# Kernel tuning notes

Hardware: AMD Instinct MI355X
Metric: run time of the kernel (lower is better)

## Reference

```python
import jax, jax.numpy as jnp
import numpy as np

D = 512
B = 8
S1 = 2048
S2 = 2048


def _rope_cos_sin(seq_len, dim, dtype=jnp.float32):
    half = dim // 2
    inv_freq = 1.0 / (10000.0 ** (jnp.arange(half, dtype=jnp.float32) / half))
    t = jnp.arange(seq_len, dtype=jnp.float32)
    freqs = jnp.outer(t, inv_freq)                      # [S, D/2]
    emb = jnp.concatenate([freqs, freqs], axis=-1)      # [S, D]
    return jnp.cos(emb).astype(dtype), jnp.sin(emb).astype(dtype)


def _rotate_half(x):
    half = x.shape[-1] // 2
    return jnp.concatenate([-x[..., half:], x[..., :half]], axis=-1)


def _apply_rope(x, cos, sin):
    # x: [B, S, D]; cos/sin: [S, D]
    return x * cos[None, :, :] + _rotate_half(x) * sin[None, :, :]


def setup_inputs() -> dict:
    key = jax.random.key(0)
    ks = jax.random.split(key, 12)
    s = 1.0 / np.sqrt(D)
    return {
        "h1": jax.random.normal(ks[0], (B, S1, D), dtype=jnp.float32),
        "h2": jax.random.normal(ks[1], (B, S2, D), dtype=jnp.float32),
        "Wq": jax.random.normal(ks[2], (D, D), dtype=jnp.float32) * s,
        "bq": jnp.zeros((D,), dtype=jnp.float32),
        "Wk": jax.random.normal(ks[3], (D, D), dtype=jnp.float32) * s,
        "bk": jnp.zeros((D,), dtype=jnp.float32),
        "Wv": jax.random.normal(ks[4], (D, D), dtype=jnp.float32) * s,
        "bv": jnp.zeros((D,), dtype=jnp.float32),
        "Wo": jax.random.normal(ks[5], (D, D), dtype=jnp.float32) * s,
        "bo": jnp.zeros((D,), dtype=jnp.float32),
    }


def reference(h1, h2, Wq, bq, Wk, bk, Wv, bv, Wo, bo):
    d = h1.shape[-1]
    # Linear projections (torch Linear: x @ W.T + b)
    q = jnp.einsum("bsd,ed->bse", h1, Wq) + bq
    k = jnp.einsum("bsd,ed->bse", h2, Wk) + bk
    v = jnp.einsum("bsd,ed->bse", h2, Wv) + bv
    # RoPE on full hidden dim (single head)
    cos_q, sin_q = _rope_cos_sin(q.shape[1], d)
    cos_k, sin_k = _rope_cos_sin(k.shape[1], d)
    q = _apply_rope(q, cos_q, sin_q)
    k = _apply_rope(k, cos_k, sin_k)
    # scaled dot-product attention with full score matrix (faithful to source)
    energy = jnp.einsum("bqd,bkd->bqk", q, k) / jnp.sqrt(jnp.float32(d))
    attn = jax.nn.softmax(energy, axis=-1)
    out = jnp.einsum("bqk,bkd->bqd", attn, v)
    return jnp.einsum("bsd,ed->bse", out, Wo) + bo
```

## Files before the change

kernel.cpp:

```cpp
#include <hip/hip_runtime.h>
#include <stdint.h>

#define SCALE_E 0.044194173824159216f
#define LOG2_10000 13.287712379549449f
#define MCONST 8.0f

typedef __bf16 bf16x8 __attribute__((ext_vector_type(8)));
typedef float  f32x4  __attribute__((ext_vector_type(4)));

#define MFMA16(a, b, c) __builtin_amdgcn_mfma_f32_16x16x32_bf16((a), (b), (c), 0, 0, 0)

__device__ __forceinline__ void gload_lds16(const void* gp, void* lp) {
  __builtin_amdgcn_global_load_lds(
      reinterpret_cast<const uint32_t __attribute__((address_space(1)))*>(
          reinterpret_cast<uintptr_t>(gp)),
      reinterpret_cast<uint32_t __attribute__((address_space(3)))*>(
          reinterpret_cast<uintptr_t>(lp)),
      16, 0, 0);
}

__global__ __launch_bounds__(256) void gemm_split(
    const float* __restrict__ A, const float* __restrict__ W,
    const float* __restrict__ bias, float* __restrict__ C, int M)
{
  __shared__ __align__(16) __bf16 Als[2 * 512 * 8];
  __shared__ __align__(16) __bf16 Wls[2 * 512 * 8];

  const int t    = threadIdx.x;
  const int lane = t & 63;
  const int w    = t >> 6;
  const int m    = lane & 15;
  const int quad = lane >> 4;
  const int mw   = w & 1;
  const int nw   = w >> 1;
  const int m0   = blockIdx.y * 128;
  const int n0   = blockIdx.x * 128;

  const float* Ap0 = A + (size_t)(m0 + w * 16 + m) * 512 + quad * 8;
  const float* Ap1 = A + (size_t)(m0 + (w + 4) * 16 + m) * 512 + quad * 8;
  const float* Wp0 = W + (size_t)(n0 + w * 16 + m) * 512 + quad * 8;
  const float* Wp1 = W + (size_t)(n0 + (w + 4) * 16 + m) * 512 + quad * 8;

  f32x4 acc[4][4] = {};

  float4 ra[4], rw_[4];
  ra[0] = *(const float4*)(Ap0);     ra[1] = *(const float4*)(Ap0 + 4);
  ra[2] = *(const float4*)(Ap1);     ra[3] = *(const float4*)(Ap1 + 4);
  rw_[0] = *(const float4*)(Wp0);    rw_[1] = *(const float4*)(Wp0 + 4);
  rw_[2] = *(const float4*)(Wp1);    rw_[3] = *(const float4*)(Wp1 + 4);

  for (int kt = 0; kt < 512; kt += 32) {
    __syncthreads();
    #pragma unroll
    for (int h = 0; h < 2; ++h) {
      int slot = t + 256 * h;
      float v[8] = {ra[2*h].x, ra[2*h].y, ra[2*h].z, ra[2*h].w,
                    ra[2*h+1].x, ra[2*h+1].y, ra[2*h+1].z, ra[2*h+1].w};
      float u[8] = {rw_[2*h].x, rw_[2*h].y, rw_[2*h].z, rw_[2*h].w,
                    rw_[2*h+1].x, rw_[2*h+1].y, rw_[2*h+1].z, rw_[2*h+1].w};
      bf16x8 ah, al, bh, bl;
      #pragma unroll
      for (int j = 0; j < 8; ++j) {
        __bf16 hv = (__bf16)v[j];
        ah[j] = hv; al[j] = (__bf16)(v[j] - (float)hv);
        __bf16 hu = (__bf16)u[j];
        bh[j] = hu; bl[j] = (__bf16)(u[j] - (float)hu);
      }
      *(bf16x8*)&Als[(size_t)slot * 8]         = ah;
      *(bf16x8*)&Als[(size_t)(512 + slot) * 8] = al;
      *(bf16x8*)&Wls[(size_t)slot * 8]         = bh;
      *(bf16x8*)&Wls[(size_t)(512 + slot) * 8] = bl;
    }
    __syncthreads();

    if (kt + 32 < 512) {
      ra[0] = *(const float4*)(Ap0 + kt + 32);  ra[1] = *(const float4*)(Ap0 + kt + 36);
      ra[2] = *(const float4*)(Ap1 + kt + 32);  ra[3] = *(const float4*)(Ap1 + kt + 36);
      rw_[0] = *(const float4*)(Wp0 + kt + 32); rw_[1] = *(const float4*)(Wp0 + kt + 36);
      rw_[2] = *(const float4*)(Wp1 + kt + 32); rw_[3] = *(const float4*)(Wp1 + kt + 36);
    }

    bf16x8 ah[4], al[4], bh[4], bl[4];
    #pragma unroll
    for (int mt = 0; mt < 4; ++mt) {
      ah[mt] = *(const bf16x8*)&Als[(size_t)((mw * 4 + mt) * 64 + lane) * 8];
      al[mt] = *(const bf16x8*)&Als[(size_t)(512 + (mw * 4 + mt) * 64 + lane) * 8];
    }
    #pragma unroll
    for (int nt = 0; nt < 4; ++nt) {
      bh[nt] = *(const bf16x8*)&Wls[(size_t)((nw * 4 + nt) * 64 + lane) * 8];
      bl[nt] = *(const bf16x8*)&Wls[(size_t)(512 + (nw * 4 + nt) * 64 + lane) * 8];
    }
    #pragma unroll
    for (int mt = 0; mt < 4; ++mt)
      #pragma unroll
      for (int nt = 0; nt < 4; ++nt) {
        acc[mt][nt] = MFMA16(al[mt], bh[nt], acc[mt][nt]);
        acc[mt][nt] = MFMA16(ah[mt], bl[nt], acc[mt][nt]);
        acc[mt][nt] = MFMA16(ah[mt], bh[nt], acc[mt][nt]);
      }
  }

  float bv[4];
  #pragma unroll
  for (int nt = 0; nt < 4; ++nt) bv[nt] = bias[n0 + (nw * 4 + nt) * 16 + m];

  #pragma unroll
  for (int mt = 0; mt < 4; ++mt)
    #pragma unroll
    for (int r = 0; r < 4; ++r) {
      size_t row = m0 + (mw * 4 + mt) * 16 + quad * 4 + r;
      float* cp = C + row * 512 + n0;
      #pragma unroll
      for (int nt = 0; nt < 4; ++nt)
        cp[(nw * 4 + nt) * 16 + m] = acc[mt][nt][r] + bv[nt];
    }
}

__global__ __launch_bounds__(256) void rope_cast(
    const float* __restrict__ X, __bf16* __restrict__ Y, float scale)
{
  const int row = blockIdx.x;
  const int s = row & 2047;
  const int j = threadIdx.x;
  const float* p = X + (size_t)row * 512;
  __bf16* q = Y + (size_t)row * 512;
  float invf = exp2f((float)j * (-LOG2_10000 / 256.0f));
  float ang = (float)s * invf;
  float c = cosf(ang), sn = sinf(ang);
  float x1 = p[j], x2 = p[j + 256];
  q[j]       = (__bf16)((x1 * c - x2 * sn) * scale);
  q[j + 256] = (__bf16)((x2 * c + x1 * sn) * scale);
}

__global__ __launch_bounds__(256) void cast_transpose_v(
    const float* __restrict__ V, __bf16* __restrict__ Vt)
{
  __shared__ float tile[32][33];
  const int b  = blockIdx.z;
  const int s0 = blockIdx.x * 32;
  const int d0 = blockIdx.y * 32;
  const float* Vb = V + (size_t)b * 2048 * 512;
  __bf16* Vtb = Vt + (size_t)b * 512 * 2048;

  #pragma unroll
  for (int r = 0; r < 4; ++r) {
    int s = s0 + threadIdx.y + 8 * r;
    tile[threadIdx.y + 8 * r][threadIdx.x] = Vb[(size_t)s * 512 + d0 + threadIdx.x];
  }
  __syncthreads();
  #pragma unroll
  for (int r = 0; r < 4; ++r) {
    int d = d0 + threadIdx.y + 8 * r;
    Vtb[(size_t)d * 2048 + s0 + threadIdx.x] = (__bf16)tile[threadIdx.x][threadIdx.y + 8 * r];
  }
}

__global__ __launch_bounds__(512, 2) void attn_mfma(
    const __bf16* __restrict__ Qb, const __bf16* __restrict__ Kb,
    const __bf16* __restrict__ Vt, float* __restrict__ O)
{
  __shared__ __align__(16) __bf16 Kbuf[2][2048 * 8];
  __shared__ __align__(16) __bf16 Vbuf[2048 * 8];
  __shared__ __align__(16) __bf16 Ps[2048];
  __shared__ float l_sh[128];

  const int t    = threadIdx.x;
  const int b    = blockIdx.x >> 5;
  const int q0   = (blockIdx.x & 31) * 64;
  const int w    = t >> 6;
  const int lane = t & 63;
  const int m    = lane & 15;
  const int quad = lane >> 4;
  const int rw   = w >> 1;
  const int kw   = w & 1;

  const __bf16* Kbase = Kb + (size_t)b * 2048 * 512;
  const __bf16* Vbase = Vt + (size_t)b * 512 * 2048;

  const __bf16* qrow = Qb + ((size_t)b * 2048 + q0 + rw * 16 + m) * 512 + quad * 8;
  bf16x8 qf[16];
  #pragma unroll
  for (int kb = 0; kb < 16; ++kb) qf[kb] = *(const bf16x8*)(qrow + kb * 32);

  f32x4 o_acc[4][4] = {};
  float l_acc[4] = {};

  #pragma unroll
  for (int i = 0; i < 4; ++i) {
    const int j = w * 4 + i;
    gload_lds16(Kbase + (size_t)((j & 1) * 16 + m) * 512 + (j >> 1) * 32 + quad * 8,
                &Kbuf[0][(size_t)(j * 64 + lane) * 8]);
  }

  for (int kt = 0; kt < 2048; kt += 32) {
    const int cur = (kt >> 5) & 1;
    __syncthreads();

    #pragma unroll
    for (int i = 0; i < 4; ++i) {
      const int j = w * 4 + i;
      gload_lds16(Vbase + (size_t)(j * 16 + m) * 2048 + kt + quad * 8,
                  &Vbuf[(size_t)(j * 64 + lane) * 8]);
    }
    if (kt + 32 < 2048) {
      #pragma unroll
      for (int i = 0; i < 4; ++i) {
        const int j = w * 4 + i;
        gload_lds16(Kbase + (size_t)(kt + 32 + (j & 1) * 16 + m) * 512 + (j >> 1) * 32 + quad * 8,
                    &Kbuf[1 - cur][(size_t)(j * 64 + lane) * 8]);
      }
    }

    f32x4 sc0 = {0.f, 0.f, 0.f, 0.f}, sc1 = {0.f, 0.f, 0.f, 0.f};
    #pragma unroll
    for (int kb = 0; kb < 16; kb += 2) {
      bf16x8 k0 = *(const bf16x8*)&Kbuf[cur][(size_t)(((kb + 0) * 2 + kw) * 64 + lane) * 8];
      bf16x8 k1 = *(const bf16x8*)&Kbuf[cur][(size_t)(((kb + 1) * 2 + kw) * 64 + lane) * 8];
      sc0 = MFMA16(qf[kb + 0], k0, sc0);
      sc1 = MFMA16(qf[kb + 1], k1, sc1);
    }
    f32x4 sc = sc0 + sc1;

    float p0 = __expf(sc[0] - MCONST);
    float p1 = __expf(sc[1] - MCONST);
    float p2 = __expf(sc[2] - MCONST);
    float p3 = __expf(sc[3] - MCONST);
    {
      __bf16* pw = &Ps[(size_t)((rw * 4 + kw * 2 + (m >> 3)) * 16 + quad * 4) * 8 + (m & 7)];
      pw[0]  = (__bf16)p0;
      pw[8]  = (__bf16)p1;
      pw[16] = (__bf16)p2;
      pw[24] = (__bf16)p3;
    }
    float r0 = p0, r1 = p1, r2 = p2, r3 = p3;
    #pragma unroll
    for (int off = 1; off < 16; off <<= 1) {
      r0 += __shfl_xor(r0, off, 16);
      r1 += __shfl_xor(r1, off, 16);
      r2 += __shfl_xor(r2, off, 16);
      r3 += __shfl_xor(r3, off, 16);
    }
    l_acc[0] += r0; l_acc[1] += r1; l_acc[2] += r2; l_acc[3] += r3;

    __syncthreads();

    {
      bf16x8 pf0 = *(const bf16x8*)&Ps[(size_t)(0 * 64 + lane) * 8];
      bf16x8 pf1 = *(const bf16x8*)&Ps[(size_t)(1 * 64 + lane) * 8];
      bf16x8 pf2 = *(const bf16x8*)&Ps[(size_t)(2 * 64 + lane) * 8];
      bf16x8 pf3 = *(const bf16x8*)&Ps[(size_t)(3 * 64 + lane) * 8];
      #pragma unroll
      for (int dt = 0; dt < 4; ++dt) {
        bf16x8 vf = *(const bf16x8*)&Vbuf[(size_t)((w * 4 + dt) * 64 + lane) * 8];
        o_acc[0][dt] = MFMA16(pf0, vf, o_acc[0][dt]);
        o_acc[1][dt] = MFMA16(pf1, vf, o_acc[1][dt]);
        o_acc[2][dt] = MFMA16(pf2, vf, o_acc[2][dt]);
        o_acc[3][dt] = MFMA16(pf3, vf, o_acc[3][dt]);
      }
    }
  }

  if (m == 0) {
    #pragma unroll
    for (int r = 0; r < 4; ++r)
      l_sh[kw * 64 + rw * 16 + quad * 4 + r] = l_acc[r];
  }
  __syncthreads();
  #pragma unroll
  for (int rt = 0; rt < 4; ++rt) {
    float invl[4];
    #pragma unroll
    for (int r = 0; r < 4; ++r)
      invl[r] = 1.0f / (l_sh[rt * 16 + quad * 4 + r] + l_sh[64 + rt * 16 + quad * 4 + r]);
    #pragma unroll
    for (int dt = 0; dt < 4; ++dt)
      #pragma unroll
      for (int r = 0; r < 4; ++r) {
        size_t row = (size_t)b * 2048 + q0 + rt * 16 + quad * 4 + r;
        O[row * 512 + w * 64 + dt * 16 + m] = o_acc[rt][dt][r] * invl[r];
      }
  }
}

extern "C" void kernel_launch(void* const* d_in, const int* in_sizes, int n_in,
                              void* d_out, int out_size, void* d_ws, size_t ws_size,
                              hipStream_t stream)
{
  const float* h1 = (const float*)d_in[0];
  const float* h2 = (const float*)d_in[1];
  const float* Wq = (const float*)d_in[2];
  const float* bq = (const float*)d_in[3];
  const float* Wk = (const float*)d_in[4];
  const float* bk = (const float*)d_in[5];
  const float* Wv = (const float*)d_in[6];
  const float* bv = (const float*)d_in[7];
  const float* Wo = (const float*)d_in[8];
  const float* bo = (const float*)d_in[9];
  float* out = (float*)d_out;

  const size_t MB = 1024 * 1024;

  float*  Qf  = (float*)d_ws;
  float*  Kf  = (float*)((char*)d_ws + 32 * MB);
  float*  O2  = (float*)((char*)d_ws + 16 * MB);
  __bf16* Vtb = (__bf16*)d_ws;
  __bf16* Qbb = (__bf16*)((char*)d_ws + 64 * MB);
  __bf16* Kbb = (__bf16*)((char*)d_ws + 80 * MB);
  float*  Vf  = out;

  const int M = 8 * 2048;
  dim3 gG(4, M / 128);

  gemm_split<<<gG, 256, 0, stream>>>(h1, Wq, bq, Qf, M);
  gemm_split<<<gG, 256, 0, stream>>>(h2, Wk, bk, Kf, M);
  gemm_split<<<gG, 256, 0, stream>>>(h2, Wv, bv, Vf, M);
  rope_cast<<<M, 256, 0, stream>>>(Qf, Qbb, SCALE_E);
  rope_cast<<<M, 256, 0, stream>>>(Kf, Kbb, 1.0f);
  cast_transpose_v<<<dim3(64, 16, 8), dim3(32, 8), 0, stream>>>(Vf, Vtb);
  attn_mfma<<<256, 512, 0, stream>>>(Qbb, Kbb, Vtb, O2);
  gemm_split<<<gG, 256, 0, stream>>>(O2, Wo, bo, out, M);
}
```

Before: 447.3 us.

## Widen attention key tile to 64 and single-buffer K with post-sync prefetch

Doubles the key tile per iteration from 32 to 64, halving the number of loop iterations and block-wide barriers. K is now single-buffered: the next tile is loaded after the second barrier and overlaps with the PV MFMAs, replacing double buffering. Each wave now computes two 16-column score tiles that share one Q fragment. LDS use per block rises (roughly 144KB), which may block two blocks per CU at launch bounds (512,2), and the next K load has less time to hide its latency.

```diff
diff --git a/kernel.cpp b/kernel.cpp
--- a/kernel.cpp
+++ b/kernel.cpp
@@ -160,9 +160,9 @@
     const __bf16* __restrict__ Qb, const __bf16* __restrict__ Kb,
     const __bf16* __restrict__ Vt, float* __restrict__ O)
 {
-  __shared__ __align__(16) __bf16 Kbuf[2][2048 * 8];
-  __shared__ __align__(16) __bf16 Vbuf[2048 * 8];
-  __shared__ __align__(16) __bf16 Ps[2048];
+  __shared__ __align__(16) __bf16 Kbuf[4096 * 8];
+  __shared__ __align__(16) __bf16 Vbuf[4096 * 8];
+  __shared__ __align__(16) __bf16 Ps[4096];
   __shared__ float l_sh[128];
 
   const int t    = threadIdx.x;
@@ -173,7 +173,7 @@
   const int m    = lane & 15;
   const int quad = lane >> 4;
   const int rw   = w >> 1;
-  const int kw   = w & 1;
+  const int kp   = w & 1;
 
   const __bf16* Kbase = Kb + (size_t)b * 2048 * 512;
   const __bf16* Vbase = Vt + (size_t)b * 512 * 2048;
@@ -187,76 +187,82 @@
   float l_acc[4] = {};
 
   #pragma unroll
-  for (int i = 0; i < 4; ++i) {
-    const int j = w * 4 + i;
-    gload_lds16(Kbase + (size_t)((j & 1) * 16 + m) * 512 + (j >> 1) * 32 + quad * 8,
-                &Kbuf[0][(size_t)(j * 64 + lane) * 8]);
-  }
-
-  for (int kt = 0; kt < 2048; kt += 32) {
-    const int cur = (kt >> 5) & 1;
+  for (int i = 0; i < 8; ++i) {
+    const int j = w * 8 + i;
+    gload_lds16(Kbase + (size_t)((j & 3) * 16 + m) * 512 + (j >> 2) * 32 + quad * 8,
+                &Kbuf[(size_t)(j * 64 + lane) * 8]);
+  }
+
+  for (int kt = 0; kt < 2048; kt += 64) {
     __syncthreads();
 
     #pragma unroll
-    for (int i = 0; i < 4; ++i) {
-      const int j = w * 4 + i;
-      gload_lds16(Vbase + (size_t)(j * 16 + m) * 2048 + kt + quad * 8,
+    for (int i = 0; i < 8; ++i) {
+      const int j = w * 8 + i;
+      gload_lds16(Vbase + (size_t)((j >> 1) * 16 + m) * 2048 + kt + (j & 1) * 32 + quad * 8,
                   &Vbuf[(size_t)(j * 64 + lane) * 8]);
     }
-    if (kt + 32 < 2048) {
-      #pragma unroll
-      for (int i = 0; i < 4; ++i) {
-        const int j = w * 4 + i;
-        gload_lds16(Kbase + (size_t)(kt + 32 + (j & 1) * 16 + m) * 512 + (j >> 1) * 32 + quad * 8,
-                    &Kbuf[1 - cur][(size_t)(j * 64 + lane) * 8]);
-      }
-    }
 
     f32x4 sc0 = {0.f, 0.f, 0.f, 0.f}, sc1 = {0.f, 0.f, 0.f, 0.f};
     #pragma unroll
-    for (int kb = 0; kb < 16; kb += 2) {
-      bf16x8 k0 = *(const bf16x8*)&Kbuf[cur][(size_t)(((kb + 0) * 2 + kw) * 64 + lane) * 8];
-      bf16x8 k1 = *(const bf16x8*)&Kbuf[cur][(size_t)(((kb + 1) * 2 + kw) * 64 + lane) * 8];
-      sc0 = MFMA16(qf[kb + 0], k0, sc0);
-      sc1 = MFMA16(qf[kb + 1], k1, sc1);
-    }
-    f32x4 sc = sc0 + sc1;
-
-    float p0 = __expf(sc[0] - MCONST);
-    float p1 = __expf(sc[1] - MCONST);
-    float p2 = __expf(sc[2] - MCONST);
-    float p3 = __expf(sc[3] - MCONST);
-    {
-      __bf16* pw = &Ps[(size_t)((rw * 4 + kw * 2 + (m >> 3)) * 16 + quad * 4) * 8 + (m & 7)];
-      pw[0]  = (__bf16)p0;
-      pw[8]  = (__bf16)p1;
-      pw[16] = (__bf16)p2;
-      pw[24] = (__bf16)p3;
-    }
-    float r0 = p0, r1 = p1, r2 = p2, r3 = p3;
-    #pragma unroll
-    for (int off = 1; off < 16; off <<= 1) {
-      r0 += __shfl_xor(r0, off, 16);
-      r1 += __shfl_xor(r1, off, 16);
-      r2 += __shfl_xor(r2, off, 16);
-      r3 += __shfl_xor(r3, off, 16);
-    }
-    l_acc[0] += r0; l_acc[1] += r1; l_acc[2] += r2; l_acc[3] += r3;
+    for (int kb = 0; kb < 16; ++kb) {
+      bf16x8 k0 = *(const bf16x8*)&Kbuf[(size_t)((kb * 4 + kp * 2 + 0) * 64 + lane) * 8];
+      bf16x8 k1 = *(const bf16x8*)&Kbuf[(size_t)((kb * 4 + kp * 2 + 1) * 64 + lane) * 8];
+      sc0 = MFMA16(qf[kb], k0, sc0);
+      sc1 = MFMA16(qf[kb], k1, sc1);
+    }
+
+    #pragma unroll
+    for (int g = 0; g < 2; ++g) {
+      const int kg = kp * 2 + g;
+      f32x4 sc = g ? sc1 : sc0;
+      float p0 = __expf(sc[0] - MCONST);
+      float p1 = __expf(sc[1] - MCONST);
+      float p2 = __expf(sc[2] - MCONST);
+      float p3 = __expf(sc[3] - MCONST);
+      {
+        __bf16* pw = &Ps[(size_t)(((rw * 2 + (kg >> 1)) * 4 + ((kg & 1) * 2 + (m >> 3))) * 16
+                                  + quad * 4) * 8 + (m & 7)];
+        pw[0]  = (__bf16)p0;
+        pw[8]  = (__bf16)p1;
+        pw[16] = (__bf16)p2;
+        pw[24] = (__bf16)p3;
+      }
+      float r0 = p0, r1 = p1, r2 = p2, r3 = p3;
+      #pragma unroll
+      for (int off = 1; off < 16; off <<= 1) {
+        r0 += __shfl_xor(r0, off, 16);
+        r1 += __shfl_xor(r1, off, 16);
+        r2 += __shfl_xor(r2, off, 16);
+        r3 += __shfl_xor(r3, off, 16);
+      }
+      l_acc[0] += r0; l_acc[1] += r1; l_acc[2] += r2; l_acc[3] += r3;
+    }
 
     __syncthreads();
 
-    {
-      bf16x8 pf0 = *(const bf16x8*)&Ps[(size_t)(0 * 64 + lane) * 8];
-      bf16x8 pf1 = *(const bf16x8*)&Ps[(size_t)(1 * 64 + lane) * 8];
-      bf16x8 pf2 = *(const bf16x8*)&Ps[(size_t)(2 * 64 + lane) * 8];
-      bf16x8 pf3 = *(const bf16x8*)&Ps[(size_t)(3 * 64 + lane) * 8];
+    if (kt + 64 < 2048) {
+      #pragma unroll
+      for (int i = 0; i < 8; ++i) {
+        const int j = w * 8 + i;
+        gload_lds16(Kbase + (size_t)(kt + 64 + (j & 3) * 16 + m) * 512 + (j >> 2) * 32 + quad * 8,
+                    &Kbuf[(size_t)(j * 64 + lane) * 8]);
+      }
+    }
+
+    #pragma unroll
+    for (int kh = 0; kh < 2; ++kh) {
+      bf16x8 pf[4];
+      #pragma unroll
+      for (int rg = 0; rg < 4; ++rg)
+        pf[rg] = *(const bf16x8*)&Ps[(size_t)((rg * 2 + kh) * 64 + lane) * 8];
       #pragma unroll
       for (int dt = 0; dt < 4; ++dt) {
-        bf16x8 vf = *(const bf16x8*)&Vbuf[(size_t)((w * 4 + dt) * 64 + lane) * 8];
-        o_acc[0][dt] = MFMA16(pf0, vf, o_acc[0][dt]);
-        o_acc[1][dt] = MFMA16(pf1, vf, o_acc[1][dt]);
-        o_acc[2][dt] = MFMA16(pf2, vf, o_acc[2][dt]);
-        o_acc[3][dt] = MFMA16(pf3, vf, o_acc[3][dt]);
+        bf16x8 vf = *(const bf16x8*)&Vbuf[(size_t)(((w * 4 + dt) * 2 + kh) * 64 + lane) * 8];
+        o_acc[0][dt] = MFMA16(pf[0], vf, o_acc[0][dt]);
+        o_acc[1][dt] = MFMA16(pf[1], vf, o_acc[1][dt]);
+        o_acc[2][dt] = MFMA16(pf[2], vf, o_acc[2][dt]);
+        o_acc[3][dt] = MFMA16(pf[3], vf, o_acc[3][dt]);
       }
     }
   }
@@ -264,7 +270,7 @@
   if (m == 0) {
     #pragma unroll
     for (int r = 0; r < 4; ++r)
-      l_sh[kw * 64 + rw * 16 + quad * 4 + r] = l_acc[r];
+      l_sh[kp * 64 + rw * 16 + quad * 4 + r] = l_acc[r];
   }
   __syncthreads();
   #pragma unroll
```

After: 414.6 us. 1.08x faster.
